# Optimization experiments

Hardware: AMD Instinct MI355X
Metric: run time of the kernel (lower is better)

## Reference

```python
import jax, jax.numpy as jnp
import numpy as np

# Static multi-scale pyramid configuration (matches src_spatial_shapes / level_start_index inputs)
LEVEL_SHAPES = [(128, 128), (64, 64), (32, 32), (16, 16)]  # (H, W) per level
NH, NL, NP = 8, 4, 4  # n_heads, n_levels, n_points
D = 256


def setup_inputs() -> dict:
    key = jax.random.key(0)
    ks = jax.random.split(key, 24)
    N, Lq = 4, 8192
    Lin = sum(h * w for h, w in LEVEL_SHAPES)  # 21760
    d_ff = 4 * D
    inp = {
        "tgt": jax.random.normal(ks[0], (N, Lq, D), jnp.float32),
        "query_pos": jax.random.normal(ks[1], (N, Lq, D), jnp.float32),
        "reference_points": jax.random.uniform(ks[2], (N, Lq, NL, 2), jnp.float32),
        "src": jax.random.normal(ks[3], (N, Lin, D), jnp.float32),
        "src_spatial_shapes": jnp.array(LEVEL_SHAPES, dtype=jnp.int64),
        "level_start_index": jnp.array(np.cumsum([0] + [h * w for h, w in LEVEL_SHAPES[:-1]]), dtype=jnp.int64),
        "src_padding_mask": jnp.zeros((N, Lin), dtype=bool),
        # MSDeformAttn params
        "W_off": jax.random.normal(ks[4], (D, NH * NL * NP * 2), jnp.float32) * 0.01,
        "b_off": jax.random.normal(ks[5], (NH * NL * NP * 2,), jnp.float32) * 0.01,
        "W_attn": jax.random.normal(ks[6], (D, NH * NL * NP), jnp.float32) * 0.02,
        "b_attn": jnp.zeros((NH * NL * NP,), jnp.float32),
        "W_val": jax.random.normal(ks[7], (D, D), jnp.float32) * 0.02,
        "b_val": jnp.zeros((D,), jnp.float32),
        "W_out": jax.random.normal(ks[8], (D, D), jnp.float32) * 0.02,
        "b_out": jnp.zeros((D,), jnp.float32),
        # LN + MLP params
        "ln1_g": jnp.ones((D,), jnp.float32),
        "ln1_b": jnp.zeros((D,), jnp.float32),
        "W_fc1": jax.random.normal(ks[9], (D, d_ff), jnp.float32) * 0.02,
        "b_fc1": jnp.zeros((d_ff,), jnp.float32),
        "W_fc2": jax.random.normal(ks[10], (d_ff, D), jnp.float32) * 0.02,
        "b_fc2": jnp.zeros((D,), jnp.float32),
        "ln2_g": jnp.ones((D,), jnp.float32),
        "ln2_b": jnp.zeros((D,), jnp.float32),
    }
    return inp


def _layer_norm(x, g, b, eps=1e-5):
    x32 = x.astype(jnp.float32)
    m = x32.mean(-1, keepdims=True)
    v = x32.var(-1, keepdims=True)
    return (((x32 - m) * jax.lax.rsqrt(v + eps)) * g + b).astype(x.dtype)


def _sample_level(value_flat, H, W, loc):
    # value_flat: [N, H*W, NH, hd]; loc: [N, Lq, NH, NP, 2] in [0,1]
    # torch.grid_sample align_corners=False, padding_mode='zeros'
    x = loc[..., 0] * W - 0.5
    y = loc[..., 1] * H - 0.5
    x0 = jnp.floor(x)
    y0 = jnp.floor(y)
    dx, dy = x - x0, y - y0
    N, Lq, nh, P = x.shape
    hd = value_flat.shape[-1]
    corners = [
        (x0, y0, (1.0 - dx) * (1.0 - dy)),
        (x0 + 1.0, y0, dx * (1.0 - dy)),
        (x0, y0 + 1.0, (1.0 - dx) * dy),
        (x0 + 1.0, y0 + 1.0, dx * dy),
    ]
    out = jnp.zeros((N, Lq * P, nh, hd), value_flat.dtype)
    for cx, cy, w in corners:
        valid = (cx >= 0) & (cx <= W - 1) & (cy >= 0) & (cy <= H - 1)
        ix = jnp.clip(cx, 0, W - 1).astype(jnp.int32)
        iy = jnp.clip(cy, 0, H - 1).astype(jnp.int32)
        idx = (iy * W + ix).transpose(0, 1, 3, 2).reshape(N, Lq * P, nh)[..., None]
        v = jnp.take_along_axis(value_flat, idx, axis=1)  # [N, Lq*P, NH, hd]
        ww = (w * valid).transpose(0, 1, 3, 2).reshape(N, Lq * P, nh)[..., None]
        out = out + v * ww
    return out.reshape(N, Lq, P, nh, hd)  # [N, Lq, NP, NH, hd]


def reference(tgt, query_pos, reference_points, src, src_spatial_shapes,
              level_start_index, src_padding_mask,
              W_off, b_off, W_attn, b_attn, W_val, b_val, W_out, b_out,
              ln1_g, ln1_b, W_fc1, b_fc1, W_fc2, b_fc2, ln2_g, ln2_b):
    N, Lq, _ = tgt.shape
    hd = D // NH
    q = tgt + query_pos

    # value projection + padding mask
    value = src @ W_val + b_val
    value = jnp.where(src_padding_mask[..., None], 0.0, value)
    value = value.reshape(N, -1, NH, hd)

    # sampling offsets and attention weights
    off = (q @ W_off + b_off).reshape(N, Lq, NH, NL, NP, 2)
    aw = (q @ W_attn + b_attn).reshape(N, Lq, NH, NL * NP)
    aw = jax.nn.softmax(aw, axis=-1).reshape(N, Lq, NH, NL, NP)

    # normalize offsets by (W, H) per level
    normalizer = jnp.array([[w, h] for (h, w) in LEVEL_SHAPES], jnp.float32)  # [NL, 2]
    loc = reference_points[:, :, None, :, None, :] + off / normalizer[None, None, None, :, None, :]

    out = jnp.zeros((N, Lq, NH, hd), value.dtype)
    start = 0
    for l, (H, W) in enumerate(LEVEL_SHAPES):
        vflat = value[:, start:start + H * W]
        start += H * W
        sampled = _sample_level(vflat, H, W, loc[:, :, :, l])  # [N, Lq, NP, NH, hd]
        w_l = aw[:, :, :, l].transpose(0, 1, 3, 2)[..., None]  # [N, Lq, NP, NH, 1]
        out = out + (sampled * w_l).sum(axis=2)
    attn_out = out.reshape(N, Lq, D) @ W_out + b_out

    # residual + LN + MLP (named 'gelu' but is ReLU in source) + LN
    x = _layer_norm(tgt + attn_out, ln1_g, ln1_b)
    h = jax.nn.relu(x @ W_fc1 + b_fc1) @ W_fc2 + b_fc2
    x = _layer_norm(x + h, ln2_g, ln2_b)
    return x
```

## Files before the change

kernel.cpp:

```cpp
#include <hip/hip_runtime.h>
#include <hip/hip_bf16.h>

constexpr int NB    = 4;
constexpr int LQ    = 8192;
constexpr int DM    = 256;
constexpr int NHEAD = 8;
constexpr int HD    = 32;
constexpr int LIN   = 21760;
constexpr int DFF   = 1024;
constexpr int MQ    = NB * LQ;
constexpr int MV    = NB * LIN;

typedef __attribute__((ext_vector_type(8))) short short8;
typedef __attribute__((ext_vector_type(4))) float f32x4;

__device__ __forceinline__ ushort f2b(float f) {
  union { __hip_bfloat16 h; ushort u; } c;
  c.h = __float2bfloat16(f);
  return c.u;
}
__device__ __forceinline__ float b2f(ushort u) {
  return __uint_as_float((unsigned int)u << 16);
}

__device__ __forceinline__ void load_lds16(const ushort* g, ushort* l) {
  __builtin_amdgcn_global_load_lds(
      (const __attribute__((address_space(1))) void*)g,
      (__attribute__((address_space(3))) void*)l, 16, 0, 0);
}

__global__ __launch_bounds__(256) void k_packall(
    const float* __restrict__ Wval, const float* __restrict__ Woff,
    const float* __restrict__ Wattn, const float* __restrict__ Wout,
    const float* __restrict__ W1, const float* __restrict__ W2,
    ushort* __restrict__ wvalP, ushort* __restrict__ wqP,
    ushort* __restrict__ woutP, ushort* __restrict__ w1P,
    ushort* __restrict__ w2P) {
  const int bid = blockIdx.x;
  const float* W; ushort* P; int K, Nsrc, n_base, local;
  if (bid < 64)       { W = Wval;  P = wvalP; K = 256;  Nsrc = 256;  n_base = 0;   local = bid; }
  else if (bid < 128) { W = Woff;  P = wqP;   K = 256;  Nsrc = 256;  n_base = 0;   local = bid - 64; }
  else if (bid < 160) { W = Wattn; P = wqP;   K = 256;  Nsrc = 128;  n_base = 256; local = bid - 128; }
  else if (bid < 224) { W = Wout;  P = woutP; K = 256;  Nsrc = 256;  n_base = 0;   local = bid - 160; }
  else if (bid < 480) { W = W1;    P = w1P;   K = 256;  Nsrc = 1024; n_base = 0;   local = bid - 224; }
  else                { W = W2;    P = w2P;   K = 1024; Nsrc = 256;  n_base = 0;   local = bid - 480; }
  const int kb = local % (K >> 5), nb = local / (K >> 5);
  const int k0 = kb * 32, n0 = nb * 32;

  __shared__ float T[32][33];
  const int t = threadIdx.x;
  {
    const int r = t >> 3, c4 = t & 7;
    const float4 v = *reinterpret_cast<const float4*>(
        &W[(size_t)(k0 + r) * Nsrc + n0 + c4 * 4]);
    T[r][c4 * 4 + 0] = v.x;
    T[r][c4 * 4 + 1] = v.y;
    T[r][c4 * 4 + 2] = v.z;
    T[r][c4 * 4 + 3] = v.w;
  }
  __syncthreads();
  const int dn = t >> 3, q = t & 7;
  const int n = n_base + n0 + dn;
  const int k = k0 + q * 4;
  const int Tt = n >> 4, fr = n & 15, kg = (k >> 3) & 3;
  const int idx = Tt * (K >> 5) + (k >> 5);
  ushort4 o;
  o.x = f2b(T[q * 4 + 0][dn]);
  o.y = f2b(T[q * 4 + 1][dn]);
  o.z = f2b(T[q * 4 + 2][dn]);
  o.w = f2b(T[q * 4 + 3][dn]);
  *reinterpret_cast<ushort4*>(&P[(size_t)idx * 512 + (kg * 16 + fr) * 8 + (k & 7)]) = o;
}

__global__ __launch_bounds__(256) void k_gemmA(
    const float* __restrict__ Af, const ushort* __restrict__ BP,
    const float* __restrict__ bias,
    ushort* __restrict__ out0, int M, int N, int K) {
  __shared__ __align__(16) ushort SMEM[17408];
  ushort* As = SMEM;
  const int m0 = blockIdx.x * 128, n0 = blockIdx.y * 128;
  const int t = threadIdx.x, w = t >> 6, l = t & 63;
  const int wr = (w >> 1) * 64, wc = (w & 1) * 64;
  const int fr = l & 15, kg = l >> 4;
  const int lrow = l >> 3;
  const int sg = (l & 7) ^ lrow;
  const int Kg = K >> 5;

  f32x4 acc[4][4];
#pragma unroll
  for (int i = 0; i < 4; ++i)
#pragma unroll
    for (int j = 0; j < 4; ++j) acc[i][j] = f32x4{0.f, 0.f, 0.f, 0.f};

  for (int k0 = 0; k0 < K; k0 += 64) {
    float4 fa[4][2];
#pragma unroll
    for (int i = 0; i < 4; ++i) {
      const float* ap = Af + (size_t)(m0 + i * 32 + w * 8 + lrow) * K + k0 + sg * 8;
      fa[i][0] = *reinterpret_cast<const float4*>(ap);
      fa[i][1] = *reinterpret_cast<const float4*>(ap + 4);
    }
    __syncthreads();
#pragma unroll
    for (int i = 0; i < 4; ++i) {
      uint4 u;
      u.x = (unsigned int)f2b(fa[i][0].x) | ((unsigned int)f2b(fa[i][0].y) << 16);
      u.y = (unsigned int)f2b(fa[i][0].z) | ((unsigned int)f2b(fa[i][0].w) << 16);
      u.z = (unsigned int)f2b(fa[i][1].x) | ((unsigned int)f2b(fa[i][1].y) << 16);
      u.w = (unsigned int)f2b(fa[i][1].z) | ((unsigned int)f2b(fa[i][1].w) << 16);
      *reinterpret_cast<uint4*>(As + i * 2048 + w * 512 + l * 8) = u;
    }
    __syncthreads();
#pragma unroll
    for (int kk = 0; kk < 2; ++kk) {
      short8 a[4], b[4];
#pragma unroll
      for (int i = 0; i < 4; ++i)
        a[i] = *reinterpret_cast<const short8*>(
            &As[(wr + i * 16 + fr) * 64 + ((kk * 4 + kg) ^ (fr & 7)) * 8]);
#pragma unroll
      for (int i = 0; i < 4; ++i)
        b[i] = *reinterpret_cast<const short8*>(
            BP + ((size_t)((n0 >> 4) + (w & 1) * 4 + i) * Kg + (k0 >> 5) + kk) * 512 + l * 8);
#pragma unroll
      for (int mi = 0; mi < 4; ++mi)
#pragma unroll
        for (int ni = 0; ni < 4; ++ni)
          acc[mi][ni] = __builtin_amdgcn_mfma_f32_16x16x32_bf16(
              b[ni], a[mi], acc[mi][ni], 0, 0, 0);
    }
  }

  ushort (*LC)[136] = (ushort(*)[136])SMEM;
  __syncthreads();
#pragma unroll
  for (int ni = 0; ni < 4; ++ni) {
    const float4 bv = *reinterpret_cast<const float4*>(&bias[n0 + wc + ni * 16 + kg * 4]);
#pragma unroll
    for (int mi = 0; mi < 4; ++mi) {
      ushort4 p;
      p.x = f2b(acc[mi][ni][0] + bv.x);
      p.y = f2b(acc[mi][ni][1] + bv.y);
      p.z = f2b(acc[mi][ni][2] + bv.z);
      p.w = f2b(acc[mi][ni][3] + bv.w);
      *reinterpret_cast<ushort4*>(&LC[wr + mi * 16 + fr][wc + ni * 16 + kg * 4]) = p;
    }
  }
  __syncthreads();
  const int c = t & 15, rb = t >> 4;
#pragma unroll
  for (int i = 0; i < 8; ++i) {
    const int r = rb + i * 16;
    const uint4 vv = *reinterpret_cast<const uint4*>(&LC[r][c * 8]);
    *reinterpret_cast<uint4*>(out0 + (size_t)(m0 + r) * N + n0 + c * 8) = vv;
  }
}

__global__ __launch_bounds__(256) void k_qproj(
    const float* __restrict__ tgt, const float* __restrict__ qpos,
    const ushort* __restrict__ BP, const float* __restrict__ boff,
    const float* __restrict__ battn,
    ushort* __restrict__ offb, float* __restrict__ awb) {
  __shared__ __align__(16) ushort SMEM[8704];
  __shared__ __align__(16) ushort LY[64][136];
  ushort* As = SMEM;
  const int m0 = blockIdx.x * 64;
  const int t = threadIdx.x, w = t >> 6, l = t & 63;
  const int fr = l & 15, kg = l >> 4;
  const int lrow = l >> 3;
  const int sg = (l & 7) ^ lrow;

  f32x4 acc[4][6];
#pragma unroll
  for (int i = 0; i < 4; ++i)
#pragma unroll
    for (int j = 0; j < 6; ++j) acc[i][j] = f32x4{0.f, 0.f, 0.f, 0.f};

  for (int k0 = 0; k0 < 256; k0 += 64) {
    float4 fa[2][2];
#pragma unroll
    for (int i = 0; i < 2; ++i) {
      const int row = m0 + i * 32 + w * 8 + lrow;
      const float* ap = tgt + (size_t)row * 256 + k0 + sg * 8;
      const float* ap2 = qpos + (size_t)row * 256 + k0 + sg * 8;
      fa[i][0] = *reinterpret_cast<const float4*>(ap);
      fa[i][1] = *reinterpret_cast<const float4*>(ap + 4);
      const float4 x = *reinterpret_cast<const float4*>(ap2);
      const float4 y = *reinterpret_cast<const float4*>(ap2 + 4);
      fa[i][0].x += x.x; fa[i][0].y += x.y; fa[i][0].z += x.z; fa[i][0].w += x.w;
      fa[i][1].x += y.x; fa[i][1].y += y.y; fa[i][1].z += y.z; fa[i][1].w += y.w;
    }
    __syncthreads();
#pragma unroll
    for (int i = 0; i < 2; ++i) {
      uint4 u;
      u.x = (unsigned int)f2b(fa[i][0].x) | ((unsigned int)f2b(fa[i][0].y) << 16);
      u.y = (unsigned int)f2b(fa[i][0].z) | ((unsigned int)f2b(fa[i][0].w) << 16);
      u.z = (unsigned int)f2b(fa[i][1].x) | ((unsigned int)f2b(fa[i][1].y) << 16);
      u.w = (unsigned int)f2b(fa[i][1].z) | ((unsigned int)f2b(fa[i][1].w) << 16);
      *reinterpret_cast<uint4*>(As + i * 2048 + w * 512 + l * 8) = u;
    }
    __syncthreads();
#pragma unroll
    for (int kk = 0; kk < 2; ++kk) {
      short8 a[4], b[6];
#pragma unroll
      for (int i = 0; i < 4; ++i)
        a[i] = *reinterpret_cast<const short8*>(
            &As[(i * 16 + fr) * 64 + ((kk * 4 + kg) ^ (fr & 7)) * 8]);
#pragma unroll
      for (int i = 0; i < 6; ++i)
        b[i] = *reinterpret_cast<const short8*>(
            BP + ((size_t)(w * 6 + i) * 8 + (k0 >> 5) + kk) * 512 + l * 8);
#pragma unroll
      for (int mi = 0; mi < 4; ++mi)
#pragma unroll
        for (int ni = 0; ni < 6; ++ni)
          acc[mi][ni] = __builtin_amdgcn_mfma_f32_16x16x32_bf16(
              b[ni], a[mi], acc[mi][ni], 0, 0, 0);
    }
  }

#pragma unroll
  for (int p = 0; p < 3; ++p) {
    __syncthreads();
#pragma unroll
    for (int ni = 0; ni < 6; ++ni) {
      const int cb = w * 96 + ni * 16;
      if (cb >= p * 128 && cb < p * 128 + 128) {
        const int col = cb + kg * 4;
        float4 bv;
        if (col < 256) bv = *reinterpret_cast<const float4*>(&boff[col]);
        else           bv = *reinterpret_cast<const float4*>(&battn[col - 256]);
#pragma unroll
        for (int mi = 0; mi < 4; ++mi) {
          ushort4 q;
          q.x = f2b(acc[mi][ni][0] + bv.x);
          q.y = f2b(acc[mi][ni][1] + bv.y);
          q.z = f2b(acc[mi][ni][2] + bv.z);
          q.w = f2b(acc[mi][ni][3] + bv.w);
          *reinterpret_cast<ushort4*>(&LY[mi * 16 + fr][cb - p * 128 + kg * 4]) = q;
        }
      }
    }
    __syncthreads();
    if (p < 2) {
      const int c = t & 15, rb = t >> 4;
#pragma unroll
      for (int i = 0; i < 4; ++i) {
        const int r = rb + i * 16;
        const uint4 vv = *reinterpret_cast<const uint4*>(&LY[r][c * 8]);
        *reinterpret_cast<uint4*>(offb + (size_t)(m0 + r) * 256 + p * 128 + c * 8) = vv;
      }
    } else {
#pragma unroll
      for (int gi = 0; gi < 2; ++gi) {
        const int g = t + gi * 256;
        const int row = g >> 3, hh = g & 7;
        const uint4 u0 = *reinterpret_cast<const uint4*>(&LY[row][hh * 16]);
        const uint4 u1 = *reinterpret_cast<const uint4*>(&LY[row][hh * 16 + 8]);
        const unsigned int uw[8] = {u0.x, u0.y, u0.z, u0.w, u1.x, u1.y, u1.z, u1.w};
        float e[16];
#pragma unroll
        for (int i = 0; i < 4; ++i) {
          e[2*i]   = __uint_as_float(uw[i] << 16);
          e[2*i+1] = __uint_as_float(uw[i] & 0xffff0000u);
          e[8+2*i]   = __uint_as_float(uw[4+i] << 16);
          e[8+2*i+1] = __uint_as_float(uw[4+i] & 0xffff0000u);
        }
        float mx = e[0];
#pragma unroll
        for (int i = 1; i < 16; ++i) mx = fmaxf(mx, e[i]);
        float s = 0.f;
#pragma unroll
        for (int i = 0; i < 16; ++i) { e[i] = __expf(e[i] - mx); s += e[i]; }
        const float inv = 1.f / s;
        float* o = awb + (size_t)(m0 + row) * 128 + hh * 16;
#pragma unroll
        for (int i = 0; i < 4; ++i) {
          float4 q;
          q.x = e[4*i]*inv; q.y = e[4*i+1]*inv; q.z = e[4*i+2]*inv; q.w = e[4*i+3]*inv;
          *reinterpret_cast<float4*>(o + 4*i) = q;
        }
      }
    }
  }
}

__global__ __launch_bounds__(256) void k_outln(
    const ushort* __restrict__ A, const ushort* __restrict__ BP,
    const float* __restrict__ bias, const float* __restrict__ res,
    const float* __restrict__ g, const float* __restrict__ bvec,
    ushort* __restrict__ out, int K) {
  __shared__ __align__(16) ushort SMEM[17408];
  ushort* As = SMEM;
  const int m0 = blockIdx.x * 64;
  const int t = threadIdx.x, w = t >> 6, l = t & 63;
  const int wc = w * 64;
  const int fr = l & 15, kg = l >> 4;
  const int lrow = l >> 3;
  const int sg = (l & 7) ^ lrow;
  const int Kg = K >> 5;

  f32x4 acc[4][4];
#pragma unroll
  for (int i = 0; i < 4; ++i)
#pragma unroll
    for (int j = 0; j < 4; ++j) acc[i][j] = f32x4{0.f, 0.f, 0.f, 0.f};

  for (int k0 = 0; k0 < K; k0 += 64) {
    __syncthreads();
#pragma unroll
    for (int i = 0; i < 2; ++i)
      load_lds16(A + (size_t)(m0 + i * 32 + w * 8 + lrow) * K + k0 + sg * 8,
                 As + i * 2048 + w * 512);
    __syncthreads();
#pragma unroll
    for (int kk = 0; kk < 2; ++kk) {
      short8 a[4], b[4];
#pragma unroll
      for (int i = 0; i < 4; ++i)
        a[i] = *reinterpret_cast<const short8*>(
            &As[(i * 16 + fr) * 64 + ((kk * 4 + kg) ^ (fr & 7)) * 8]);
#pragma unroll
      for (int i = 0; i < 4; ++i)
        b[i] = *reinterpret_cast<const short8*>(
            BP + ((size_t)(w * 4 + i) * Kg + (k0 >> 5) + kk) * 512 + l * 8);
#pragma unroll
      for (int mi = 0; mi < 4; ++mi)
#pragma unroll
        for (int ni = 0; ni < 4; ++ni)
          acc[mi][ni] = __builtin_amdgcn_mfma_f32_16x16x32_bf16(
              b[ni], a[mi], acc[mi][ni], 0, 0, 0);
    }
  }

  ushort (*LY)[272] = (ushort(*)[272])SMEM;
  __syncthreads();
#pragma unroll
  for (int ni = 0; ni < 4; ++ni) {
    const float4 bv = *reinterpret_cast<const float4*>(&bias[wc + ni * 16 + kg * 4]);
#pragma unroll
    for (int mi = 0; mi < 4; ++mi) {
      ushort4 p;
      p.x = f2b(acc[mi][ni][0] + bv.x);
      p.y = f2b(acc[mi][ni][1] + bv.y);
      p.z = f2b(acc[mi][ni][2] + bv.z);
      p.w = f2b(acc[mi][ni][3] + bv.w);
      *reinterpret_cast<ushort4*>(&LY[mi * 16 + fr][wc + ni * 16 + kg * 4]) = p;
    }
  }
  __syncthreads();

  const int c = t & 31, rb = t >> 5;
#pragma unroll
  for (int i = 0; i < 8; ++i) {
    const int r = rb + i * 8;
    const uint4 yy = *reinterpret_cast<const uint4*>(&LY[r][c * 8]);
    const unsigned int yw[4] = {yy.x, yy.y, yy.z, yy.w};
    float v[8];
#pragma unroll
    for (int j = 0; j < 4; ++j) {
      v[2 * j]     = __uint_as_float(yw[j] << 16);
      v[2 * j + 1] = __uint_as_float(yw[j] & 0xffff0000u);
    }
    const float* rp = res + (size_t)(m0 + r) * 256 + c * 8;
    const float4 r0 = *reinterpret_cast<const float4*>(rp);
    const float4 r1 = *reinterpret_cast<const float4*>(rp + 4);
    v[0] += r0.x; v[1] += r0.y; v[2] += r0.z; v[3] += r0.w;
    v[4] += r1.x; v[5] += r1.y; v[6] += r1.z; v[7] += r1.w;
    float s = 0.f, ss = 0.f;
#pragma unroll
    for (int j = 0; j < 8; ++j) { s += v[j]; ss += v[j] * v[j]; }
#pragma unroll
    for (int o = 1; o < 32; o <<= 1) {
      s  += __shfl_xor(s, o);
      ss += __shfl_xor(ss, o);
    }
    const float m = s * (1.f / 256.f);
    const float inv = rsqrtf(ss * (1.f / 256.f) - m * m + 1e-5f);
    const float4 g0 = *reinterpret_cast<const float4*>(&g[c * 8]);
    const float4 g1 = *reinterpret_cast<const float4*>(&g[c * 8 + 4]);
    const float4 b0 = *reinterpret_cast<const float4*>(&bvec[c * 8]);
    const float4 b1 = *reinterpret_cast<const float4*>(&bvec[c * 8 + 4]);
    uint4 u;
    u.x = (unsigned int)f2b((v[0] - m) * inv * g0.x + b0.x) |
          ((unsigned int)f2b((v[1] - m) * inv * g0.y + b0.y) << 16);
    u.y = (unsigned int)f2b((v[2] - m) * inv * g0.z + b0.z) |
          ((unsigned int)f2b((v[3] - m) * inv * g0.w + b0.w) << 16);
    u.z = (unsigned int)f2b((v[4] - m) * inv * g1.x + b1.x) |
          ((unsigned int)f2b((v[5] - m) * inv * g1.y + b1.y) << 16);
    u.w = (unsigned int)f2b((v[6] - m) * inv * g1.z + b1.z) |
          ((unsigned int)f2b((v[7] - m) * inv * g1.w + b1.w) << 16);
    *reinterpret_cast<uint4*>(out + (size_t)(m0 + r) * 256 + c * 8) = u;
  }
}

__global__ __launch_bounds__(256) void k_ffn(
    const ushort* __restrict__ X, const ushort* __restrict__ W1P,
    const float* __restrict__ bb1, const ushort* __restrict__ W2P,
    const float* __restrict__ bb2, const float* __restrict__ g2,
    const float* __restrict__ b2v, float* __restrict__ out) {
  __shared__ __align__(16) ushort SMEM[24576];
  ushort* Xs = SMEM;
  ushort* Hs = SMEM + 16384;
  const int m0 = blockIdx.x * 64;
  const int t = threadIdx.x, w = t >> 6, l = t & 63;
  const int fr = l & 15, kg = l >> 4;

#pragma unroll
  for (int i = 0; i < 8; ++i) {
    const int gi = w * 8 + i;
    const int row = gi * 2 + (l >> 5);
    load_lds16(X + (size_t)(m0 + row) * 256 + (((l & 31) ^ (row & 7)) * 8),
               Xs + gi * 512);
  }
  __syncthreads();

  f32x4 acc2[4][4];
#pragma unroll
  for (int i = 0; i < 4; ++i)
#pragma unroll
    for (int j = 0; j < 4; ++j) acc2[i][j] = f32x4{0.f, 0.f, 0.f, 0.f};

  for (int c = 0; c < 8; ++c) {
    f32x4 acc1[4][2];
#pragma unroll
    for (int i = 0; i < 4; ++i)
#pragma unroll
      for (int j = 0; j < 2; ++j) acc1[i][j] = f32x4{0.f, 0.f, 0.f, 0.f};
#pragma unroll
    for (int ks = 0; ks < 8; ++ks) {
      short8 a[4], b[2];
#pragma unroll
      for (int mi = 0; mi < 4; ++mi)
        a[mi] = *reinterpret_cast<const short8*>(
            &Xs[(mi * 16 + fr) * 256 + ((ks * 4 + kg) ^ (fr & 7)) * 8]);
#pragma unroll
      for (int ni = 0; ni < 2; ++ni)
        b[ni] = *reinterpret_cast<const short8*>(
            W1P + ((size_t)(c * 8 + w * 2 + ni) * 8 + ks) * 512 + l * 8);
#pragma unroll
      for (int mi = 0; mi < 4; ++mi)
#pragma unroll
        for (int ni = 0; ni < 2; ++ni)
          acc1[mi][ni] = __builtin_amdgcn_mfma_f32_16x16x32_bf16(
              b[ni], a[mi], acc1[mi][ni], 0, 0, 0);
    }
    __syncthreads();
#pragma unroll
    for (int ni = 0; ni < 2; ++ni) {
      const float4 bv = *reinterpret_cast<const float4*>(
          &bb1[c * 128 + w * 32 + ni * 16 + kg * 4]);
#pragma unroll
      for (int mi = 0; mi < 4; ++mi) {
        const int row = mi * 16 + fr;
        const int gcol = w * 4 + ni * 2 + (kg >> 1);
        ushort4 p;
        p.x = f2b(fmaxf(acc1[mi][ni][0] + bv.x, 0.f));
        p.y = f2b(fmaxf(acc1[mi][ni][1] + bv.y, 0.f));
        p.z = f2b(fmaxf(acc1[mi][ni][2] + bv.z, 0.f));
        p.w = f2b(fmaxf(acc1[mi][ni][3] + bv.w, 0.f));
        *reinterpret_cast<ushort4*>(
            &Hs[row * 128 + ((gcol ^ (fr & 7)) * 8) + (kg & 1) * 4]) = p;
      }
    }
    __syncthreads();
#pragma unroll
    for (int ks2 = 0; ks2 < 4; ++ks2) {
      short8 a2[4], b2[4];
#pragma unroll
      for (int mi = 0; mi < 4; ++mi)
        a2[mi] = *reinterpret_cast<const short8*>(
            &Hs[(mi * 16 + fr) * 128 + ((ks2 * 4 + kg) ^ (fr & 7)) * 8]);
#pragma unroll
      for (int ni = 0; ni < 4; ++ni)
        b2[ni] = *reinterpret_cast<const short8*>(
            W2P + ((size_t)(w * 4 + ni) * 32 + c * 4 + ks2) * 512 + l * 8);
#pragma unroll
      for (int mi = 0; mi < 4; ++mi)
#pragma unroll
        for (int ni = 0; ni < 4; ++ni)
          acc2[mi][ni] = __builtin_amdgcn_mfma_f32_16x16x32_bf16(
              b2[ni], a2[mi], acc2[mi][ni], 0, 0, 0);
    }
  }

#pragma unroll
  for (int ni = 0; ni < 4; ++ni) {
    const int colb = w * 64 + ni * 16 + kg * 4;
    const float4 bv = *reinterpret_cast<const float4*>(&bb2[colb]);
    const int g = w * 8 + ni * 2 + (kg >> 1);
#pragma unroll
    for (int mi = 0; mi < 4; ++mi) {
      const int row = mi * 16 + fr;
      const ushort4 xr = *reinterpret_cast<const ushort4*>(
          &Xs[row * 256 + ((g ^ (fr & 7)) * 8) + (kg & 1) * 4]);
      acc2[mi][ni][0] += bv.x + b2f(xr.x);
      acc2[mi][ni][1] += bv.y + b2f(xr.y);
      acc2[mi][ni][2] += bv.z + b2f(xr.z);
      acc2[mi][ni][3] += bv.w + b2f(xr.w);
    }
  }
  __syncthreads();

  ushort (*LY)[272] = (ushort(*)[272])SMEM;
#pragma unroll
  for (int ni = 0; ni < 4; ++ni) {
#pragma unroll
    for (int mi = 0; mi < 4; ++mi) {
      ushort4 p;
      p.x = f2b(acc2[mi][ni][0]);
      p.y = f2b(acc2[mi][ni][1]);
      p.z = f2b(acc2[mi][ni][2]);
      p.w = f2b(acc2[mi][ni][3]);
      *reinterpret_cast<ushort4*>(&LY[mi * 16 + fr][w * 64 + ni * 16 + kg * 4]) = p;
    }
  }
  __syncthreads();

  const int cc = t & 31, rb = t >> 5;
#pragma unroll
  for (int i = 0; i < 8; ++i) {
    const int r = rb + i * 8;
    const uint4 yy = *reinterpret_cast<const uint4*>(&LY[r][cc * 8]);
    const unsigned int yw[4] = {yy.x, yy.y, yy.z, yy.w};
    float v[8];
#pragma unroll
    for (int j = 0; j < 4; ++j) {
      v[2 * j]     = __uint_as_float(yw[j] << 16);
      v[2 * j + 1] = __uint_as_float(yw[j] & 0xffff0000u);
    }
    float s = 0.f, ss = 0.f;
#pragma unroll
    for (int j = 0; j < 8; ++j) { s += v[j]; ss += v[j] * v[j]; }
#pragma unroll
    for (int o = 1; o < 32; o <<= 1) {
      s  += __shfl_xor(s, o);
      ss += __shfl_xor(ss, o);
    }
    const float m = s * (1.f / 256.f);
    const float inv = rsqrtf(ss * (1.f / 256.f) - m * m + 1e-5f);
    const float4 g0 = *reinterpret_cast<const float4*>(&g2[cc * 8]);
    const float4 g1 = *reinterpret_cast<const float4*>(&g2[cc * 8 + 4]);
    const float4 b0 = *reinterpret_cast<const float4*>(&b2v[cc * 8]);
    const float4 b1 = *reinterpret_cast<const float4*>(&b2v[cc * 8 + 4]);
    float* opp = out + (size_t)(m0 + r) * 256 + cc * 8;
    float4 q0, q1;
    q0.x = (v[0] - m) * inv * g0.x + b0.x;
    q0.y = (v[1] - m) * inv * g0.y + b0.y;
    q0.z = (v[2] - m) * inv * g0.z + b0.z;
    q0.w = (v[3] - m) * inv * g0.w + b0.w;
    q1.x = (v[4] - m) * inv * g1.x + b1.x;
    q1.y = (v[5] - m) * inv * g1.y + b1.y;
    q1.z = (v[6] - m) * inv * g1.z + b1.z;
    q1.w = (v[7] - m) * inv * g1.w + b1.w;
    *reinterpret_cast<float4*>(opp) = q0;
    *reinterpret_cast<float4*>(opp + 4) = q1;
  }
}

__global__ __launch_bounds__(256) void k_sample(
    const float* __restrict__ refp, const ushort* __restrict__ offb,
    const float* __restrict__ awb, const ushort* __restrict__ value,
    ushort* __restrict__ pre) {
  const int bid = ((blockIdx.x & 7) << 9) | (blockIdx.x >> 3);
  const int tid = bid * 256 + threadIdx.x;
  const int cg = tid & 3;
  const int h  = (tid >> 2) & 7;
  const int nq = tid >> 5;
  const int n  = nq >> 13;

  const float4 r01 = *reinterpret_cast<const float4*>(refp + (size_t)nq * 8);
  const float4 r23 = *reinterpret_cast<const float4*>(refp + (size_t)nq * 8 + 4);
  const float rxs[4] = {r01.x, r01.z, r23.x, r23.z};
  const float rys[4] = {r01.y, r01.w, r23.y, r23.w};
  const ushort* op = offb + (size_t)nq * 256 + h * 32;
  const float*  ap = awb + (size_t)nq * 128 + h * 16;
  const ushort* vb = value + (size_t)n * LIN * DM + h * HD + cg * 8;

  float acc[8];
#pragma unroll
  for (int j = 0; j < 8; ++j) acc[j] = 0.f;

  const int WL[4] = {128, 64, 32, 16};
  const int ST[4] = {0, 16384, 20480, 21504};

#pragma unroll
  for (int lvl = 0; lvl < 4; ++lvl) {
    const int Wl = WL[lvl];
    const float fW = (float)Wl;
    const float invW = 1.f / fW;
    const float rx = rxs[lvl], ry = rys[lvl];
    const ushort* vl = vb + (size_t)ST[lvl] * DM;
    const uint4 ov = *reinterpret_cast<const uint4*>(op + lvl * 8);
    const float4 a4 = *reinterpret_cast<const float4*>(ap + lvl * 4);
    const unsigned int ow[4] = {ov.x, ov.y, ov.z, ov.w};
    const float aa[4] = {a4.x, a4.y, a4.z, a4.w};
#pragma unroll
    for (int p = 0; p < 4; ++p) {
      const float ox = __uint_as_float(ow[p] << 16);
      const float oy = __uint_as_float(ow[p] & 0xffff0000u);
      const float xx = (rx + ox * invW) * fW - 0.5f;
      const float yy = (ry + oy * invW) * fW - 0.5f;
      const float a = aa[p];
      const float x0 = floorf(xx), y0 = floorf(yy);
      const float dx = xx - x0, dy = yy - y0;
      const bool vx0 = (x0 >= 0.f) && (x0 <= fW - 1.f);
      const bool vx1 = (x0 + 1.f >= 0.f) && (x0 + 1.f <= fW - 1.f);
      const bool vy0 = (y0 >= 0.f) && (y0 <= fW - 1.f);
      const bool vy1 = (y0 + 1.f >= 0.f) && (y0 + 1.f <= fW - 1.f);
      const int ix0 = min(max((int)x0, 0), Wl - 1);
      const int ix1 = min(max((int)x0 + 1, 0), Wl - 1);
      const int iy0 = min(max((int)y0, 0), Wl - 1);
      const int iy1 = min(max((int)y0 + 1, 0), Wl - 1);
      const float w00 = (vx0 && vy0) ? (1.f - dx) * (1.f - dy) * a : 0.f;
      const float w10 = (vx1 && vy0) ? dx * (1.f - dy) * a : 0.f;
      const float w01 = (vx0 && vy1) ? (1.f - dx) * dy * a : 0.f;
      const float w11 = (vx1 && vy1) ? dx * dy * a : 0.f;
      const ushort* r0 = vl + (size_t)iy0 * Wl * DM;
      const ushort* r1 = vl + (size_t)iy1 * Wl * DM;
      const uint4 u00 = *reinterpret_cast<const uint4*>(r0 + ix0 * DM);
      const uint4 u10 = *reinterpret_cast<const uint4*>(r0 + ix1 * DM);
      const uint4 u01 = *reinterpret_cast<const uint4*>(r1 + ix0 * DM);
      const uint4 u11 = *reinterpret_cast<const uint4*>(r1 + ix1 * DM);
      const unsigned int uu00[4] = {u00.x, u00.y, u00.z, u00.w};
      const unsigned int uu10[4] = {u10.x, u10.y, u10.z, u10.w};
      const unsigned int uu01[4] = {u01.x, u01.y, u01.z, u01.w};
      const unsigned int uu11[4] = {u11.x, u11.y, u11.z, u11.w};
#pragma unroll
      for (int i = 0; i < 4; ++i) {
        acc[2 * i]     += __uint_as_float(uu00[i] << 16) * w00;
        acc[2 * i + 1] += __uint_as_float(uu00[i] & 0xffff0000u) * w00;
        acc[2 * i]     += __uint_as_float(uu10[i] << 16) * w10;
        acc[2 * i + 1] += __uint_as_float(uu10[i] & 0xffff0000u) * w10;
        acc[2 * i]     += __uint_as_float(uu01[i] << 16) * w01;
        acc[2 * i + 1] += __uint_as_float(uu01[i] & 0xffff0000u) * w01;
        acc[2 * i]     += __uint_as_float(uu11[i] << 16) * w11;
        acc[2 * i + 1] += __uint_as_float(uu11[i] & 0xffff0000u) * w11;
      }
    }
  }

  uint4 o;
  o.x = (unsigned int)f2b(acc[0]) | ((unsigned int)f2b(acc[1]) << 16);
  o.y = (unsigned int)f2b(acc[2]) | ((unsigned int)f2b(acc[3]) << 16);
  o.z = (unsigned int)f2b(acc[4]) | ((unsigned int)f2b(acc[5]) << 16);
  o.w = (unsigned int)f2b(acc[6]) | ((unsigned int)f2b(acc[7]) << 16);
  *reinterpret_cast<uint4*>(pre + (size_t)nq * DM + h * HD + cg * 8) = o;
}

extern "C" void kernel_launch(void* const* d_in, const int* in_sizes, int n_in,
                              void* d_out, int out_size, void* d_ws, size_t ws_size,
                              hipStream_t stream) {
  const float* tgt   = (const float*)d_in[0];
  const float* qpos  = (const float*)d_in[1];
  const float* refp  = (const float*)d_in[2];
  const float* src   = (const float*)d_in[3];
  const float* Woff  = (const float*)d_in[7];
  const float* boff  = (const float*)d_in[8];
  const float* Wattn = (const float*)d_in[9];
  const float* battn = (const float*)d_in[10];
  const float* Wval  = (const float*)d_in[11];
  const float* bval  = (const float*)d_in[12];
  const float* Wout  = (const float*)d_in[13];
  const float* bout  = (const float*)d_in[14];
  const float* g1    = (const float*)d_in[15];
  const float* b1    = (const float*)d_in[16];
  const float* W1    = (const float*)d_in[17];
  const float* bb1   = (const float*)d_in[18];
  const float* W2    = (const float*)d_in[19];
  const float* bb2   = (const float*)d_in[20];
  const float* g2    = (const float*)d_in[21];
  const float* b2v   = (const float*)d_in[22];
  float* out = (float*)d_out;

  char* ws = (char*)d_ws;
  ushort* offb   = (ushort*)(ws + 0);
  ushort* valueb = (ushort*)(ws + 44564480);
  ushort* preb   = (ushort*)(ws + 89128960);
  float*  awb    = (float*)(ws + 105906176);
  ushort* xb     = (ushort*)(ws + 0);
  ushort* wvalP  = (ushort*)(ws + 156237824);
  ushort* wqP    = wvalP + 65536;
  ushort* woutP  = wqP + 98304;
  ushort* w1P    = woutP + 65536;
  ushort* w2P    = w1P + 262144;

  hipLaunchKernelGGL(k_packall, dim3(736), dim3(256), 0, stream,
                     Wval, Woff, Wattn, Wout, W1, W2,
                     wvalP, wqP, woutP, w1P, w2P);

  hipLaunchKernelGGL(k_gemmA, dim3(MV / 128, 2), dim3(256), 0, stream,
                     src, wvalP, bval, valueb, MV, DM, DM);

  hipLaunchKernelGGL(k_qproj, dim3(MQ / 64), dim3(256), 0, stream,
                     tgt, qpos, wqP, boff, battn, offb, awb);

  hipLaunchKernelGGL(k_sample, dim3(MQ * NHEAD * 4 / 256), dim3(256), 0, stream,
                     refp, offb, awb, valueb, preb);

  hipLaunchKernelGGL(k_outln, dim3(MQ / 64), dim3(256), 0, stream,
                     preb, woutP, bout, tgt, g1, b1, xb, DM);

  hipLaunchKernelGGL(k_ffn, dim3(MQ / 64), dim3(256), 0, stream,
                     xb, w1P, bb1, w2P, bb2, g2, b2v, out);
}
```

Measured before the change: 216.1 us.

## Fuse sampling into output-projection LN kernel and merge value/query projections

Merges the value-projection GEMM and the query projection into one launch that dispatches by block index, so the two independent GEMMs can run concurrently. Fuses deformable bilinear sampling into the output-projection+LayerNorm kernel: the sampled 64x256 tile is written to swizzled LDS and fed straight to the MFMA GEMM, removing the bf16 intermediate write and re-read in global memory. It also folds the offset normalisation into a precomputed scale. The trade-off is lower sampling parallelism per block (each thread handles 8 queries serially) and larger LDS use, which may reduce occupancy.

```diff
diff --git a/kernel.cpp b/kernel.cpp
--- a/kernel.cpp
+++ b/kernel.cpp
@@ -72,19 +72,18 @@
   *reinterpret_cast<ushort4*>(&P[(size_t)idx * 512 + (kg * 16 + fr) * 8 + (k & 7)]) = o;
 }
 
-__global__ __launch_bounds__(256) void k_gemmA(
-    const float* __restrict__ Af, const ushort* __restrict__ BP,
-    const float* __restrict__ bias,
-    ushort* __restrict__ out0, int M, int N, int K) {
-  __shared__ __align__(16) ushort SMEM[17408];
+__device__ __forceinline__ void value_path(
+    ushort* SMEM, int bid, const float* __restrict__ Af,
+    const ushort* __restrict__ BP, const float* __restrict__ bias,
+    ushort* __restrict__ out0) {
+  constexpr int K = 256, N = 256;
   ushort* As = SMEM;
-  const int m0 = blockIdx.x * 128, n0 = blockIdx.y * 128;
+  const int m0 = (bid % 680) * 128, n0 = (bid / 680) * 128;
   const int t = threadIdx.x, w = t >> 6, l = t & 63;
   const int wr = (w >> 1) * 64, wc = (w & 1) * 64;
   const int fr = l & 15, kg = l >> 4;
   const int lrow = l >> 3;
   const int sg = (l & 7) ^ lrow;
-  const int Kg = K >> 5;
 
   f32x4 acc[4][4];
 #pragma unroll
@@ -121,7 +120,7 @@
 #pragma unroll
       for (int i = 0; i < 4; ++i)
         b[i] = *reinterpret_cast<const short8*>(
-            BP + ((size_t)((n0 >> 4) + (w & 1) * 4 + i) * Kg + (k0 >> 5) + kk) * 512 + l * 8);
+            BP + ((size_t)((n0 >> 4) + (w & 1) * 4 + i) * 8 + (k0 >> 5) + kk) * 512 + l * 8);
 #pragma unroll
       for (int mi = 0; mi < 4; ++mi)
 #pragma unroll
@@ -156,15 +155,14 @@
   }
 }
 
-__global__ __launch_bounds__(256) void k_qproj(
-    const float* __restrict__ tgt, const float* __restrict__ qpos,
-    const ushort* __restrict__ BP, const float* __restrict__ boff,
-    const float* __restrict__ battn,
+__device__ __forceinline__ void qproj_path(
+    ushort* SMEM, int bid, const float* __restrict__ tgt,
+    const float* __restrict__ qpos, const ushort* __restrict__ BP,
+    const float* __restrict__ boff, const float* __restrict__ battn,
     ushort* __restrict__ offb, float* __restrict__ awb) {
-  __shared__ __align__(16) ushort SMEM[8704];
-  __shared__ __align__(16) ushort LY[64][136];
   ushort* As = SMEM;
-  const int m0 = blockIdx.x * 64;
+  ushort (*LY)[136] = (ushort(*)[136])(SMEM + 4096);
+  const int m0 = bid * 64;
   const int t = threadIdx.x, w = t >> 6, l = t & 63;
   const int fr = l & 15, kg = l >> 4;
   const int lrow = l >> 3;
@@ -287,56 +285,145 @@
   }
 }
 
-__global__ __launch_bounds__(256) void k_outln(
-    const ushort* __restrict__ A, const ushort* __restrict__ BP,
-    const float* __restrict__ bias, const float* __restrict__ res,
-    const float* __restrict__ g, const float* __restrict__ bvec,
-    ushort* __restrict__ out, int K) {
+__global__ __launch_bounds__(256) void k_vq(
+    const float* __restrict__ src, const ushort* __restrict__ wvalP,
+    const float* __restrict__ bval, ushort* __restrict__ valueb,
+    const float* __restrict__ tgt, const float* __restrict__ qpos,
+    const ushort* __restrict__ wqP, const float* __restrict__ boff,
+    const float* __restrict__ battn, ushort* __restrict__ offb,
+    float* __restrict__ awb) {
   __shared__ __align__(16) ushort SMEM[17408];
-  ushort* As = SMEM;
-  const int m0 = blockIdx.x * 64;
-  const int t = threadIdx.x, w = t >> 6, l = t & 63;
-  const int wc = w * 64;
-  const int fr = l & 15, kg = l >> 4;
-  const int lrow = l >> 3;
-  const int sg = (l & 7) ^ lrow;
-  const int Kg = K >> 5;
-
+  if (blockIdx.x < 1360)
+    value_path(SMEM, blockIdx.x, src, wvalP, bval, valueb);
+  else
+    qproj_path(SMEM, blockIdx.x - 1360, tgt, qpos, wqP, boff, battn, offb, awb);
+}
+
+__global__ __launch_bounds__(256) void k_sampout(
+    const float* __restrict__ refp, const ushort* __restrict__ offb,
+    const float* __restrict__ awb, const ushort* __restrict__ value,
+    const ushort* __restrict__ BP, const float* __restrict__ bias,
+    const float* __restrict__ res, const float* __restrict__ g,
+    const float* __restrict__ bvec, ushort* __restrict__ out) {
+  __shared__ __align__(16) ushort SMEM[64 * 272];
+  ushort* Xs = SMEM;
+  const int bid = ((blockIdx.x & 7) << 6) | (blockIdx.x >> 3);
+  const int m0 = bid * 64;
+  const int t = threadIdx.x;
+  const int cg = t & 3, h = (t >> 2) & 7, qb = t >> 5;
+  const int n = m0 >> 13;
+  const ushort* vb = value + (size_t)n * LIN * DM + h * HD + cg * 8;
+
+  const int WL[4] = {128, 64, 32, 16};
+  const int ST[4] = {0, 16384, 20480, 21504};
+
+#pragma unroll
+  for (int gq = 0; gq < 8; ++gq) {
+    const int q = qb + gq * 8;
+    const int nq = m0 + q;
+    const float4 r01 = *reinterpret_cast<const float4*>(refp + (size_t)nq * 8);
+    const float4 r23 = *reinterpret_cast<const float4*>(refp + (size_t)nq * 8 + 4);
+    const float fxs[4] = {r01.x * 128.f - 0.5f, r01.z * 64.f - 0.5f,
+                          r23.x * 32.f - 0.5f,  r23.z * 16.f - 0.5f};
+    const float fys[4] = {r01.y * 128.f - 0.5f, r01.w * 64.f - 0.5f,
+                          r23.y * 32.f - 0.5f,  r23.w * 16.f - 0.5f};
+    const ushort* op = offb + (size_t)nq * 256 + h * 32;
+    const float*  ap = awb + (size_t)nq * 128 + h * 16;
+
+    float acc[8];
+#pragma unroll
+    for (int j = 0; j < 8; ++j) acc[j] = 0.f;
+
+#pragma unroll
+    for (int lvl = 0; lvl < 4; ++lvl) {
+      const int Wl = WL[lvl];
+      const float fW = (float)Wl;
+      const ushort* vl = vb + (size_t)ST[lvl] * DM;
+      const uint4 ov = *reinterpret_cast<const uint4*>(op + lvl * 8);
+      const float4 a4 = *reinterpret_cast<const float4*>(ap + lvl * 4);
+      const unsigned int ow[4] = {ov.x, ov.y, ov.z, ov.w};
+      const float aa[4] = {a4.x, a4.y, a4.z, a4.w};
+#pragma unroll
+      for (int p = 0; p < 4; ++p) {
+        const float xx = fxs[lvl] + __uint_as_float(ow[p] << 16);
+        const float yy = fys[lvl] + __uint_as_float(ow[p] & 0xffff0000u);
+        const float a = aa[p];
+        const float x0 = floorf(xx), y0 = floorf(yy);
+        const float dx = xx - x0, dy = yy - y0;
+        const bool vx0 = (x0 >= 0.f) && (x0 <= fW - 1.f);
+        const bool vx1 = (x0 + 1.f >= 0.f) && (x0 + 1.f <= fW - 1.f);
+        const bool vy0 = (y0 >= 0.f) && (y0 <= fW - 1.f);
+        const bool vy1 = (y0 + 1.f >= 0.f) && (y0 + 1.f <= fW - 1.f);
+        const int ix0 = min(max((int)x0, 0), Wl - 1);
+        const int ix1 = min(max((int)x0 + 1, 0), Wl - 1);
+        const int iy0 = min(max((int)y0, 0), Wl - 1);
+        const int iy1 = min(max((int)y0 + 1, 0), Wl - 1);
+        const float w00 = (vx0 && vy0) ? (1.f - dx) * (1.f - dy) * a : 0.f;
+        const float w10 = (vx1 && vy0) ? dx * (1.f - dy) * a : 0.f;
+        const float w01 = (vx0 && vy1) ? (1.f - dx) * dy * a : 0.f;
+        const float w11 = (vx1 && vy1) ? dx * dy * a : 0.f;
+        const ushort* r0 = vl + (size_t)iy0 * Wl * DM;
+        const ushort* r1 = vl + (size_t)iy1 * Wl * DM;
+        const uint4 u00 = *reinterpret_cast<const uint4*>(r0 + ix0 * DM);
+        const uint4 u10 = *reinterpret_cast<const uint4*>(r0 + ix1 * DM);
+        const uint4 u01 = *reinterpret_cast<const uint4*>(r1 + ix0 * DM);
+        const uint4 u11 = *reinterpret_cast<const uint4*>(r1 + ix1 * DM);
+        const unsigned int uu00[4] = {u00.x, u00.y, u00.z, u00.w};
+        const unsigned int uu10[4] = {u10.x, u10.y, u10.z, u10.w};
+        const unsigned int uu01[4] = {u01.x, u01.y, u01.z, u01.w};
+        const unsigned int uu11[4] = {u11.x, u11.y, u11.z, u11.w};
+#pragma unroll
+        for (int i = 0; i < 4; ++i) {
+          acc[2 * i]     += __uint_as_float(uu00[i] << 16) * w00;
+          acc[2 * i + 1] += __uint_as_float(uu00[i] & 0xffff0000u) * w00;
+          acc[2 * i]     += __uint_as_float(uu10[i] << 16) * w10;
+          acc[2 * i + 1] += __uint_as_float(uu10[i] & 0xffff0000u) * w10;
+          acc[2 * i]     += __uint_as_float(uu01[i] << 16) * w01;
+          acc[2 * i + 1] += __uint_as_float(uu01[i] & 0xffff0000u) * w01;
+          acc[2 * i]     += __uint_as_float(uu11[i] << 16) * w11;
+          acc[2 * i + 1] += __uint_as_float(uu11[i] & 0xffff0000u) * w11;
+        }
+      }
+    }
+
+    uint4 o;
+    o.x = (unsigned int)f2b(acc[0]) | ((unsigned int)f2b(acc[1]) << 16);
+    o.y = (unsigned int)f2b(acc[2]) | ((unsigned int)f2b(acc[3]) << 16);
+    o.z = (unsigned int)f2b(acc[4]) | ((unsigned int)f2b(acc[5]) << 16);
+    o.w = (unsigned int)f2b(acc[6]) | ((unsigned int)f2b(acc[7]) << 16);
+    *reinterpret_cast<uint4*>(&Xs[q * 256 + (((h * 4 + cg) ^ (q & 7)) * 8)]) = o;
+  }
+  __syncthreads();
+
+  const int w = t >> 6, l = t & 63;
+  const int wc = w * 64, fr = l & 15, kg = l >> 4;
   f32x4 acc[4][4];
 #pragma unroll
   for (int i = 0; i < 4; ++i)
 #pragma unroll
     for (int j = 0; j < 4; ++j) acc[i][j] = f32x4{0.f, 0.f, 0.f, 0.f};
 
-  for (int k0 = 0; k0 < K; k0 += 64) {
-    __syncthreads();
-#pragma unroll
-    for (int i = 0; i < 2; ++i)
-      load_lds16(A + (size_t)(m0 + i * 32 + w * 8 + lrow) * K + k0 + sg * 8,
-                 As + i * 2048 + w * 512);
-    __syncthreads();
-#pragma unroll
-    for (int kk = 0; kk < 2; ++kk) {
-      short8 a[4], b[4];
-#pragma unroll
-      for (int i = 0; i < 4; ++i)
-        a[i] = *reinterpret_cast<const short8*>(
-            &As[(i * 16 + fr) * 64 + ((kk * 4 + kg) ^ (fr & 7)) * 8]);
-#pragma unroll
-      for (int i = 0; i < 4; ++i)
-        b[i] = *reinterpret_cast<const short8*>(
-            BP + ((size_t)(w * 4 + i) * Kg + (k0 >> 5) + kk) * 512 + l * 8);
-#pragma unroll
-      for (int mi = 0; mi < 4; ++mi)
-#pragma unroll
-        for (int ni = 0; ni < 4; ++ni)
-          acc[mi][ni] = __builtin_amdgcn_mfma_f32_16x16x32_bf16(
-              b[ni], a[mi], acc[mi][ni], 0, 0, 0);
-    }
-  }
+#pragma unroll
+  for (int kk = 0; kk < 8; ++kk) {
+    short8 a[4], b[4];
+#pragma unroll
+    for (int mi = 0; mi < 4; ++mi)
+      a[mi] = *reinterpret_cast<const short8*>(
+          &Xs[(mi * 16 + fr) * 256 + ((kk * 4 + kg) ^ (fr & 7)) * 8]);
+#pragma unroll
+    for (int ni = 0; ni < 4; ++ni)
+      b[ni] = *reinterpret_cast<const short8*>(
+          BP + ((size_t)(w * 4 + ni) * 8 + kk) * 512 + l * 8);
+#pragma unroll
+    for (int mi = 0; mi < 4; ++mi)
+#pragma unroll
+      for (int ni = 0; ni < 4; ++ni)
+        acc[mi][ni] = __builtin_amdgcn_mfma_f32_16x16x32_bf16(
+            b[ni], a[mi], acc[mi][ni], 0, 0, 0);
+  }
+  __syncthreads();
 
   ushort (*LY)[272] = (ushort(*)[272])SMEM;
-  __syncthreads();
 #pragma unroll
   for (int ni = 0; ni < 4; ++ni) {
     const float4 bv = *reinterpret_cast<const float4*>(&bias[wc + ni * 16 + kg * 4]);
@@ -558,96 +645,6 @@
     *reinterpret_cast<float4*>(opp) = q0;
     *reinterpret_cast<float4*>(opp + 4) = q1;
   }
-}
-
-__global__ __launch_bounds__(256) void k_sample(
-    const float* __restrict__ refp, const ushort* __restrict__ offb,
-    const float* __restrict__ awb, const ushort* __restrict__ value,
-    ushort* __restrict__ pre) {
-  const int bid = ((blockIdx.x & 7) << 9) | (blockIdx.x >> 3);
-  const int tid = bid * 256 + threadIdx.x;
-  const int cg = tid & 3;
-  const int h  = (tid >> 2) & 7;
-  const int nq = tid >> 5;
-  const int n  = nq >> 13;
-
-  const float4 r01 = *reinterpret_cast<const float4*>(refp + (size_t)nq * 8);
-  const float4 r23 = *reinterpret_cast<const float4*>(refp + (size_t)nq * 8 + 4);
-  const float rxs[4] = {r01.x, r01.z, r23.x, r23.z};
-  const float rys[4] = {r01.y, r01.w, r23.y, r23.w};
-  const ushort* op = offb + (size_t)nq * 256 + h * 32;
-  const float*  ap = awb + (size_t)nq * 128 + h * 16;
-  const ushort* vb = value + (size_t)n * LIN * DM + h * HD + cg * 8;
-
-  float acc[8];
-#pragma unroll
-  for (int j = 0; j < 8; ++j) acc[j] = 0.f;
-
-  const int WL[4] = {128, 64, 32, 16};
-  const int ST[4] = {0, 16384, 20480, 21504};
-
-#pragma unroll
-  for (int lvl = 0; lvl < 4; ++lvl) {
-    const int Wl = WL[lvl];
-    const float fW = (float)Wl;
-    const float invW = 1.f / fW;
-    const float rx = rxs[lvl], ry = rys[lvl];
-    const ushort* vl = vb + (size_t)ST[lvl] * DM;
-    const uint4 ov = *reinterpret_cast<const uint4*>(op + lvl * 8);
-    const float4 a4 = *reinterpret_cast<const float4*>(ap + lvl * 4);
-    const unsigned int ow[4] = {ov.x, ov.y, ov.z, ov.w};
-    const float aa[4] = {a4.x, a4.y, a4.z, a4.w};
-#pragma unroll
-    for (int p = 0; p < 4; ++p) {
-      const float ox = __uint_as_float(ow[p] << 16);
-      const float oy = __uint_as_float(ow[p] & 0xffff0000u);
-      const float xx = (rx + ox * invW) * fW - 0.5f;
-      const float yy = (ry + oy * invW) * fW - 0.5f;
-      const float a = aa[p];
-      const float x0 = floorf(xx), y0 = floorf(yy);
-      const float dx = xx - x0, dy = yy - y0;
-      const bool vx0 = (x0 >= 0.f) && (x0 <= fW - 1.f);
-      const bool vx1 = (x0 + 1.f >= 0.f) && (x0 + 1.f <= fW - 1.f);
-      const bool vy0 = (y0 >= 0.f) && (y0 <= fW - 1.f);
-      const bool vy1 = (y0 + 1.f >= 0.f) && (y0 + 1.f <= fW - 1.f);
-      const int ix0 = min(max((int)x0, 0), Wl - 1);
-      const int ix1 = min(max((int)x0 + 1, 0), Wl - 1);
-      const int iy0 = min(max((int)y0, 0), Wl - 1);
-      const int iy1 = min(max((int)y0 + 1, 0), Wl - 1);
-      const float w00 = (vx0 && vy0) ? (1.f - dx) * (1.f - dy) * a : 0.f;
-      const float w10 = (vx1 && vy0) ? dx * (1.f - dy) * a : 0.f;
-      const float w01 = (vx0 && vy1) ? (1.f - dx) * dy * a : 0.f;
-      const float w11 = (vx1 && vy1) ? dx * dy * a : 0.f;
-      const ushort* r0 = vl + (size_t)iy0 * Wl * DM;
-      const ushort* r1 = vl + (size_t)iy1 * Wl * DM;
-      const uint4 u00 = *reinterpret_cast<const uint4*>(r0 + ix0 * DM);
-      const uint4 u10 = *reinterpret_cast<const uint4*>(r0 + ix1 * DM);
-      const uint4 u01 = *reinterpret_cast<const uint4*>(r1 + ix0 * DM);
-      const uint4 u11 = *reinterpret_cast<const uint4*>(r1 + ix1 * DM);
-      const unsigned int uu00[4] = {u00.x, u00.y, u00.z, u00.w};
-      const unsigned int uu10[4] = {u10.x, u10.y, u10.z, u10.w};
-      const unsigned int uu01[4] = {u01.x, u01.y, u01.z, u01.w};
-      const unsigned int uu11[4] = {u11.x, u11.y, u11.z, u11.w};
-#pragma unroll
-      for (int i = 0; i < 4; ++i) {
-        acc[2 * i]     += __uint_as_float(uu00[i] << 16) * w00;
-        acc[2 * i + 1] += __uint_as_float(uu00[i] & 0xffff0000u) * w00;
-        acc[2 * i]     += __uint_as_float(uu10[i] << 16) * w10;
-        acc[2 * i + 1] += __uint_as_float(uu10[i] & 0xffff0000u) * w10;
-        acc[2 * i]     += __uint_as_float(uu01[i] << 16) * w01;
-        acc[2 * i + 1] += __uint_as_float(uu01[i] & 0xffff0000u) * w01;
-        acc[2 * i]     += __uint_as_float(uu11[i] << 16) * w11;
-        acc[2 * i + 1] += __uint_as_float(uu11[i] & 0xffff0000u) * w11;
-      }
-    }
-  }
-
-  uint4 o;
-  o.x = (unsigned int)f2b(acc[0]) | ((unsigned int)f2b(acc[1]) << 16);
-  o.y = (unsigned int)f2b(acc[2]) | ((unsigned int)f2b(acc[3]) << 16);
-  o.z = (unsigned int)f2b(acc[4]) | ((unsigned int)f2b(acc[5]) << 16);
-  o.w = (unsigned int)f2b(acc[6]) | ((unsigned int)f2b(acc[7]) << 16);
-  *reinterpret_cast<uint4*>(pre + (size_t)nq * DM + h * HD + cg * 8) = o;
 }
 
 extern "C" void kernel_launch(void* const* d_in, const int* in_sizes, int n_in,
@@ -678,7 +675,6 @@
   char* ws = (char*)d_ws;
   ushort* offb   = (ushort*)(ws + 0);
   ushort* valueb = (ushort*)(ws + 44564480);
-  ushort* preb   = (ushort*)(ws + 89128960);
   float*  awb    = (float*)(ws + 105906176);
   ushort* xb     = (ushort*)(ws + 0);
   ushort* wvalP  = (ushort*)(ws + 156237824);
@@ -691,17 +687,12 @@
                      Wval, Woff, Wattn, Wout, W1, W2,
                      wvalP, wqP, woutP, w1P, w2P);
 
-  hipLaunchKernelGGL(k_gemmA, dim3(MV / 128, 2), dim3(256), 0, stream,
-                     src, wvalP, bval, valueb, MV, DM, DM);
-
-  hipLaunchKernelGGL(k_qproj, dim3(MQ / 64), dim3(256), 0, stream,
+  hipLaunchKernelGGL(k_vq, dim3(1872), dim3(256), 0, stream,
+                     src, wvalP, bval, valueb,
                      tgt, qpos, wqP, boff, battn, offb, awb);
 
-  hipLaunchKernelGGL(k_sample, dim3(MQ * NHEAD * 4 / 256), dim3(256), 0, stream,
-                     refp, offb, awb, valueb, preb);
-
-  hipLaunchKernelGGL(k_outln, dim3(MQ / 64), dim3(256), 0, stream,
-                     preb, woutP, bout, tgt, g1, b1, xb, DM);
+  hipLaunchKernelGGL(k_sampout, dim3(MQ / 64), dim3(256), 0, stream,
+                     refp, offb, awb, valueb, woutP, bout, tgt, g1, b1, xb);
 
   hipLaunchKernelGGL(k_ffn, dim3(MQ / 64), dim3(256), 0, stream,
                      xb, w1P, bb1, w2P, bb2, g2, b2v, out);
```

Result: no change. 220.0 us (+1.8%).
